# Performance work log

Hardware: AMD Instinct MI355X
Metric: run time of the kernel (lower is better)

The kernel has to match this reference:

```python
import jax, jax.numpy as jnp
import numpy as np

N_NODES = 4096
EDGE_PROB = 0.01


def setup_inputs() -> dict:
    key = jax.random.key(0)
    kx, ka, kw = jax.random.split(key, 3)
    x = jax.random.normal(kx, (4, 32, N_NODES, 12), dtype=jnp.float32)
    u = jax.random.uniform(ka, (N_NODES, N_NODES), dtype=jnp.float32)
    adj = (u < EDGE_PROB).astype(jnp.float32)
    adj = jnp.maximum(adj, adj.T)
    weight = jax.random.normal(kw, (3, 32, 32), dtype=jnp.float32) * 0.1
    bias = jnp.zeros((32,), dtype=jnp.float32)
    return {"x": x, "adj": adj, "weight": weight, "bias": bias}


def reference(x, adj, weight, bias):
    # x: [B, c_in, N, T] -> [B, T, N, c_in] as in AdaptiveGraphConv.forward
    B, C, N, T = x.shape
    h = jnp.transpose(x, (0, 3, 2, 1))  # [B, T, N, C]
    # DenseChebConv (K=3): L = I - D^{-1/2} A D^{-1/2}, inf -> 0 for isolated nodes
    d = adj.sum(axis=-1)
    d_inv_sqrt = jnp.where(d > 0, jnp.where(d > 0, d, 1.0) ** -0.5, 0.0)
    norm_adj = d_inv_sqrt[:, None] * adj * d_inv_sqrt[None, :]
    L = jnp.eye(N, dtype=x.dtype) - norm_adj
    Tx0 = h
    Tx1 = jnp.einsum('mn,btnc->btmc', L, h)
    Tx2 = 2.0 * jnp.einsum('mn,btnc->btmc', L, Tx1) - Tx0
    out = (jnp.einsum('btnc,co->btno', Tx0, weight[0])
           + jnp.einsum('btnc,co->btno', Tx1, weight[1])
           + jnp.einsum('btnc,co->btno', Tx2, weight[2])
           + bias)
    # back to [B, c_out, N, T]
    return jnp.transpose(out, (0, 3, 2, 1))
```

## Files before the change

kernel.cpp:

```cpp
#include <hip/hip_runtime.h>

#define NN 4096
#define CC 32
#define TT 12
#define BB 4
#define BT 48
#define NC 1536
#define MAXD 192
#define FW 512
#define NCH 3
#define STP 36
#define SOP 33

typedef float f32x4 __attribute__((ext_vector_type(4)));
typedef short short8 __attribute__((ext_vector_type(8)));
typedef unsigned short ushort8 __attribute__((ext_vector_type(8)));

__device__ __forceinline__ float bf2f(unsigned short h) {
  return __uint_as_float(((unsigned int)h) << 16);
}
__device__ __forceinline__ unsigned short f2bf(float f) {
  unsigned int u = __float_as_uint(f);
  return (unsigned short)((u + 0x7FFFu + ((u >> 16) & 1u)) >> 16);
}
__device__ __forceinline__ float blo(unsigned int w) { return __uint_as_float(w << 16); }
__device__ __forceinline__ float bhi(unsigned int w) { return __uint_as_float(w & 0xFFFF0000u); }

__global__ __launch_bounds__(256) void k_build(const float* __restrict__ adj,
                                               uint2* __restrict__ edges,
                                               int* __restrict__ deg, float* __restrict__ dis) {
  __shared__ int cnt;
  int m = blockIdx.x;
  if (threadIdx.x == 0) cnt = 0;
  __syncthreads();
  unsigned int* ecol = (unsigned int*)(edges + m * MAXD);
  const uint4* row = (const uint4*)(adj + (size_t)m * NN);
  for (int i = threadIdx.x; i < NN / 4; i += 256) {
    uint4 v = row[i];
    unsigned int ws[4] = {v.x, v.y, v.z, v.w};
    #pragma unroll
    for (int k = 0; k < 4; ++k) {
      if (ws[k] != 0) {
        int p = atomicAdd(&cnt, 1);
        if (p < MAXD) ecol[p * 2] = (unsigned int)(i * 4 + k);
      }
    }
  }
  __syncthreads();
  if (threadIdx.x == 0) {
    int d = cnt < MAXD ? cnt : MAXD;
    deg[m] = d;
    dis[m] = d > 0 ? (float)(1.0 / sqrt((double)d)) : 0.0f;
  }
}

__global__ __launch_bounds__(192) void k_wt(uint2* __restrict__ edges,
                                            const int* __restrict__ deg,
                                            int* __restrict__ degp,
                                            const float* __restrict__ dis) {
  int m = blockIdx.x;
  int j = threadIdx.x;
  int d = deg[m];
  int dp = (d + 15) & ~15;
  if (j < d) {
    unsigned int* e = (unsigned int*)(edges + m * MAXD + j);
    e[1] = __float_as_uint(dis[e[0]]);
  } else if (j < dp) {
    edges[m * MAXD + j] = make_uint2((unsigned int)m, 0u);
  }
  if (j == 0) degp[m] = dp;
}

__global__ __launch_bounds__(256) void k_trans(const float* __restrict__ x,
                                               unsigned short* __restrict__ H) {
  __shared__ unsigned short sT[192 * STP];
  int b = blockIdx.x >> 8;
  int n0 = (blockIdx.x & 255) * 16;
  int c = threadIdx.x >> 3;
  int l8 = threadIdx.x & 7;
  size_t base = ((size_t)(b * CC + c) * NN + n0) * TT;
  #pragma unroll
  for (int it = 0; it < 6; ++it) {
    int j0 = it * 32 + l8 * 4;
    float4 f = *(const float4*)(x + base + j0);
    sT[(j0 + 0) * STP + c] = f2bf(f.x);
    sT[(j0 + 1) * STP + c] = f2bf(f.y);
    sT[(j0 + 2) * STP + c] = f2bf(f.z);
    sT[(j0 + 3) * STP + c] = f2bf(f.w);
  }
  __syncthreads();
  #pragma unroll
  for (int k = 0; k < 6; ++k) {
    int p = (threadIdx.x >> 3) + 32 * k;
    int nl = p / TT, t = p - nl * TT;
    ushort4 v = *(const ushort4*)&sT[p * STP + l8 * 4];
    size_t off = ((size_t)(n0 + nl) * BT + b * TT + t) * CC + l8 * 4;
    *(ushort4*)(H + off) = v;
  }
}

__global__ __launch_bounds__(1024) void k_gather(const unsigned short* __restrict__ S,
                                                 const uint2* __restrict__ edges,
                                                 const int* __restrict__ degp,
                                                 const float* __restrict__ dis,
                                                 unsigned short* __restrict__ D) {
  int tid = threadIdx.x;
  int wid = __builtin_amdgcn_readfirstlane(tid >> 6);
  int lane = tid & 63;
  int m = blockIdx.x * 16 + wid;
  int d = degp[m];
  float dm = dis[m];
  const uint2* ep = edges + (size_t)m * MAXD;
  const unsigned short* Sy = S + blockIdx.y * FW;
  int lo2 = lane * 8;
  float a0 = 0.f, a1 = 0.f, a2 = 0.f, a3 = 0.f;
  float a4 = 0.f, a5 = 0.f, a6 = 0.f, a7 = 0.f;
  for (int e = 0; e < d; e += 8) {
    uint4 hv[8];
    float w[8];
    #pragma unroll
    for (int k = 0; k < 8; ++k) {
      uint2 ew = ep[e + k];
      w[k] = __uint_as_float(ew.y);
      hv[k] = *(const uint4*)(Sy + (int)ew.x * NC + lo2);
    }
    #pragma unroll
    for (int k = 0; k < 8; ++k) {
      float wk = w[k];
      a0 = fmaf(wk, blo(hv[k].x), a0); a1 = fmaf(wk, bhi(hv[k].x), a1);
      a2 = fmaf(wk, blo(hv[k].y), a2); a3 = fmaf(wk, bhi(hv[k].y), a3);
      a4 = fmaf(wk, blo(hv[k].z), a4); a5 = fmaf(wk, bhi(hv[k].z), a5);
      a6 = fmaf(wk, blo(hv[k].w), a6); a7 = fmaf(wk, bhi(hv[k].w), a7);
    }
  }
  int fo = blockIdx.y * FW + lo2;
  ushort8 o;
  o[0] = f2bf(dm * a0); o[1] = f2bf(dm * a1);
  o[2] = f2bf(dm * a2); o[3] = f2bf(dm * a3);
  o[4] = f2bf(dm * a4); o[5] = f2bf(dm * a5);
  o[6] = f2bf(dm * a6); o[7] = f2bf(dm * a7);
  *(ushort8*)(D + (size_t)m * NC + fo) = o;
}

__global__ __launch_bounds__(256) void k_mix(const unsigned short* __restrict__ H,
                                             const unsigned short* __restrict__ G1,
                                             const unsigned short* __restrict__ G2,
                                             const float* __restrict__ W,
                                             const float* __restrict__ bias,
                                             float* __restrict__ out) {
  __shared__ __align__(16) float sOut[192 * SOP];
  int wid = threadIdx.x >> 6, lane = threadIdx.x & 63;
  int lm = lane & 15, quad = lane >> 4;
  short8 bhf[2][3], blf[2][3];
  float bias0[2];
  for (int h = 0; h < 2; ++h)
    for (int g = 0; g < 3; ++g) {
      short8 vh, vl;
      #pragma unroll
      for (int j = 0; j < 8; ++j) {
        int r = quad * 8 + j, c = h * 16 + lm;
        float w0 = W[(0 * CC + r) * CC + c];
        float w1 = W[(1 * CC + r) * CC + c];
        float w2 = W[(2 * CC + r) * CC + c];
        float w = (g == 0) ? (w0 + w1 + w2)
                 : (g == 1) ? (-w1 - 4.f * w2)
                            : (2.f * w2);
        unsigned short hi = f2bf(w);
        vh[j] = (short)hi;
        vl[j] = (short)f2bf(w - bf2f(hi));
      }
      bhf[h][g] = vh; blf[h][g] = vl;
    }
  #pragma unroll
  for (int h = 0; h < 2; ++h) bias0[h] = bias[h * 16 + lm];
  int n0 = blockIdx.x * 4;
  #pragma unroll
  for (int tI = 0; tI < 3; ++tI) {
    int r0l = wid * BT + tI * 16;
    size_t abase = ((size_t)(n0 * BT) + r0l + lm) * CC + quad * 8;
    short8 af0 = *(const short8*)(H + abase);
    short8 af1 = *(const short8*)(G1 + abase);
    short8 af2 = *(const short8*)(G2 + abase);
    #pragma unroll
    for (int h = 0; h < 2; ++h) {
      f32x4 acc = {bias0[h], bias0[h], bias0[h], bias0[h]};
      acc = __builtin_amdgcn_mfma_f32_16x16x32_bf16(af0, bhf[h][0], acc, 0, 0, 0);
      acc = __builtin_amdgcn_mfma_f32_16x16x32_bf16(af0, blf[h][0], acc, 0, 0, 0);
      acc = __builtin_amdgcn_mfma_f32_16x16x32_bf16(af1, bhf[h][1], acc, 0, 0, 0);
      acc = __builtin_amdgcn_mfma_f32_16x16x32_bf16(af1, blf[h][1], acc, 0, 0, 0);
      acc = __builtin_amdgcn_mfma_f32_16x16x32_bf16(af2, bhf[h][2], acc, 0, 0, 0);
      acc = __builtin_amdgcn_mfma_f32_16x16x32_bf16(af2, blf[h][2], acc, 0, 0, 0);
      int o = h * 16 + lm;
      #pragma unroll
      for (int reg = 0; reg < 4; ++reg)
        sOut[(r0l + quad * 4 + reg) * SOP + o] = acc[reg];
    }
  }
  __syncthreads();
  #pragma unroll
  for (int j = 0; j < 6; ++j) {
    int idx = j * 256 + threadIdx.x;
    int bo = idx / 12;
    int fq = idx - bo * 12;
    int p0 = fq * 4;
    float v[4];
    #pragma unroll
    for (int k = 0; k < 4; ++k) {
      int p = p0 + k;
      int nl = p / TT, t = p - nl * TT;
      int b = bo >> 5, o = bo & 31;
      v[k] = sOut[(nl * BT + b * TT + t) * SOP + o];
    }
    size_t base = (((size_t)bo * NN) + n0) * TT + p0;
    *(float4*)(out + base) = make_float4(v[0], v[1], v[2], v[3]);
  }
}

extern "C" void kernel_launch(void* const* d_in, const int* in_sizes, int n_in,
                              void* d_out, int out_size, void* d_ws, size_t ws_size,
                              hipStream_t stream) {
  const float* x    = (const float*)d_in[0];
  const float* adj  = (const float*)d_in[1];
  const float* wgt  = (const float*)d_in[2];
  const float* bias = (const float*)d_in[3];
  char* ws = (char*)d_ws;
  float* dis  = (float*)ws;
  int*   deg  = (int*)(ws + 16384);
  int*   degp = (int*)(ws + 32768);
  uint2* edges = (uint2*)(ws + 49152);
  char* p = ws + 49152 + (size_t)NN * MAXD * 8;
  unsigned short* H  = (unsigned short*)p;
  unsigned short* G1 = (unsigned short*)(p + (size_t)NN * NC * 2);
  unsigned short* G2 = (unsigned short*)(p + (size_t)NN * NC * 4);

  k_build<<<NN, 256, 0, stream>>>(adj, edges, deg, dis);
  k_wt<<<NN, 192, 0, stream>>>(edges, deg, degp, dis);
  k_trans<<<1024, 256, 0, stream>>>(x, H);
  k_gather<<<dim3(NN / 16, NCH), 1024, 0, stream>>>(H, edges, degp, dis, G1);
  k_gather<<<dim3(NN / 16, NCH), 1024, 0, stream>>>(G1, edges, degp, dis, G2);
  k_mix<<<NN / 4, 256, 0, stream>>>(H, G1, G2, wgt, bias, (float*)d_out);
}
```

Measured before the change: 231.8 us.

## Merge adjacency scan and input transpose into one launch with wave-ballot compaction

Folds the adjacency-row scan and the x transpose/bf16 conversion into a single kernel whose blocks split by index into the two jobs. This removes one launch and lets the two independent memory-bound jobs run side by side. The row scan now gives each row to one 64-lane wave and builds the edge list with ballot/popcount prefix sums instead of shared-memory atomics. Edge order becomes deterministic (ascending column), and each row is scanned by one wave instead of a whole block.

Result: slower. 254.4 us (+9.7%).

```diff
diff --git a/kernel.cpp b/kernel.cpp
--- a/kernel.cpp
+++ b/kernel.cpp
@@ -26,31 +26,61 @@
 __device__ __forceinline__ float blo(unsigned int w) { return __uint_as_float(w << 16); }
 __device__ __forceinline__ float bhi(unsigned int w) { return __uint_as_float(w & 0xFFFF0000u); }
 
-__global__ __launch_bounds__(256) void k_build(const float* __restrict__ adj,
-                                               uint2* __restrict__ edges,
-                                               int* __restrict__ deg, float* __restrict__ dis) {
-  __shared__ int cnt;
-  int m = blockIdx.x;
-  if (threadIdx.x == 0) cnt = 0;
-  __syncthreads();
-  unsigned int* ecol = (unsigned int*)(edges + m * MAXD);
-  const uint4* row = (const uint4*)(adj + (size_t)m * NN);
-  for (int i = threadIdx.x; i < NN / 4; i += 256) {
-    uint4 v = row[i];
-    unsigned int ws[4] = {v.x, v.y, v.z, v.w};
-    #pragma unroll
-    for (int k = 0; k < 4; ++k) {
-      if (ws[k] != 0) {
-        int p = atomicAdd(&cnt, 1);
-        if (p < MAXD) ecol[p * 2] = (unsigned int)(i * 4 + k);
+__global__ __launch_bounds__(256) void k_build_trans(const float* __restrict__ adj,
+                                                     const float* __restrict__ x,
+                                                     uint2* __restrict__ edges,
+                                                     int* __restrict__ deg,
+                                                     float* __restrict__ dis,
+                                                     unsigned short* __restrict__ H) {
+  __shared__ unsigned short sT[192 * STP];
+  if (blockIdx.x < 1024) {
+    int wid = threadIdx.x >> 6, lane = threadIdx.x & 63;
+    int m = blockIdx.x * 4 + wid;
+    const float* row = adj + (size_t)m * NN;
+    unsigned int* ecol = (unsigned int*)(edges + m * MAXD);
+    unsigned long long ltmask = (lane == 63) ? ~0ull >> 1
+                                             : (1ull << lane) - 1ull;
+    int base = 0;
+    #pragma unroll 8
+    for (int it = 0; it < 64; ++it) {
+      float v = row[it * 64 + lane];
+      unsigned long long ball = __ballot(v != 0.0f);
+      if (v != 0.0f) {
+        int p = base + __popcll(ball & ltmask);
+        if (p < MAXD) ecol[p * 2] = (unsigned int)(it * 64 + lane);
       }
-    }
-  }
-  __syncthreads();
-  if (threadIdx.x == 0) {
-    int d = cnt < MAXD ? cnt : MAXD;
-    deg[m] = d;
-    dis[m] = d > 0 ? (float)(1.0 / sqrt((double)d)) : 0.0f;
+      base += __popcll(ball);
+    }
+    if (lane == 0) {
+      int d = base < MAXD ? base : MAXD;
+      deg[m] = d;
+      dis[m] = d > 0 ? (float)(1.0 / sqrt((double)d)) : 0.0f;
+    }
+  } else {
+    int bx = blockIdx.x - 1024;
+    int b = bx >> 8;
+    int n0 = (bx & 255) * 16;
+    int c = threadIdx.x >> 3;
+    int l8 = threadIdx.x & 7;
+    size_t base = ((size_t)(b * CC + c) * NN + n0) * TT;
+    #pragma unroll
+    for (int it = 0; it < 6; ++it) {
+      int j0 = it * 32 + l8 * 4;
+      float4 f = *(const float4*)(x + base + j0);
+      sT[(j0 + 0) * STP + c] = f2bf(f.x);
+      sT[(j0 + 1) * STP + c] = f2bf(f.y);
+      sT[(j0 + 2) * STP + c] = f2bf(f.z);
+      sT[(j0 + 3) * STP + c] = f2bf(f.w);
+    }
+    __syncthreads();
+    #pragma unroll
+    for (int k = 0; k < 6; ++k) {
+      int p = (threadIdx.x >> 3) + 32 * k;
+      int nl = p / TT, t = p - nl * TT;
+      ushort4 v = *(const ushort4*)&sT[p * STP + l8 * 4];
+      size_t off = ((size_t)(n0 + nl) * BT + b * TT + t) * CC + l8 * 4;
+      *(ushort4*)(H + off) = v;
+    }
   }
 }
 
@@ -69,34 +99,6 @@
     edges[m * MAXD + j] = make_uint2((unsigned int)m, 0u);
   }
   if (j == 0) degp[m] = dp;
-}
-
-__global__ __launch_bounds__(256) void k_trans(const float* __restrict__ x,
-                                               unsigned short* __restrict__ H) {
-  __shared__ unsigned short sT[192 * STP];
-  int b = blockIdx.x >> 8;
-  int n0 = (blockIdx.x & 255) * 16;
-  int c = threadIdx.x >> 3;
-  int l8 = threadIdx.x & 7;
-  size_t base = ((size_t)(b * CC + c) * NN + n0) * TT;
-  #pragma unroll
-  for (int it = 0; it < 6; ++it) {
-    int j0 = it * 32 + l8 * 4;
-    float4 f = *(const float4*)(x + base + j0);
-    sT[(j0 + 0) * STP + c] = f2bf(f.x);
-    sT[(j0 + 1) * STP + c] = f2bf(f.y);
-    sT[(j0 + 2) * STP + c] = f2bf(f.z);
-    sT[(j0 + 3) * STP + c] = f2bf(f.w);
-  }
-  __syncthreads();
-  #pragma unroll
-  for (int k = 0; k < 6; ++k) {
-    int p = (threadIdx.x >> 3) + 32 * k;
-    int nl = p / TT, t = p - nl * TT;
-    ushort4 v = *(const ushort4*)&sT[p * STP + l8 * 4];
-    size_t off = ((size_t)(n0 + nl) * BT + b * TT + t) * CC + l8 * 4;
-    *(ushort4*)(H + off) = v;
-  }
 }
 
 __global__ __launch_bounds__(1024) void k_gather(const unsigned short* __restrict__ S,
@@ -233,9 +235,8 @@
   unsigned short* G1 = (unsigned short*)(p + (size_t)NN * NC * 2);
   unsigned short* G2 = (unsigned short*)(p + (size_t)NN * NC * 4);
 
-  k_build<<<NN, 256, 0, stream>>>(adj, edges, deg, dis);
+  k_build_trans<<<2048, 256, 0, stream>>>(adj, x, edges, deg, dis, H);
   k_wt<<<NN, 192, 0, stream>>>(edges, deg, degp, dis);
-  k_trans<<<1024, 256, 0, stream>>>(x, H);
   k_gather<<<dim3(NN / 16, NCH), 1024, 0, stream>>>(H, edges, degp, dis, G1);
   k_gather<<<dim3(NN / 16, NCH), 1024, 0, stream>>>(G1, edges, degp, dis, G2);
   k_mix<<<NN / 4, 256, 0, stream>>>(H, G1, G2, wgt, bias, (float*)d_out);
```

## Fuse second gather with channel-mix MFMA and merge build/transpose launches

Applied to the files above, without the earlier changes.

Merges the adjacency-build and input-transpose kernels into one launch, split by block index. Fuses the second sparse gather with the Chebyshev weight-mix MFMA, so each wave keeps its G2 row in shared memory and writes the final output directly. This removes the G2 round-trip through global memory and two launches. In exchange every gather block recomputes the bf16 hi/lo weight fragments, and the output stores become strided per node instead of the previous coalesced transpose through shared memory.

Measured after the change: 302.5 us. 1.3x slower.

```diff
diff --git a/kernel.cpp b/kernel.cpp
--- a/kernel.cpp
+++ b/kernel.cpp
@@ -10,7 +10,6 @@
 #define FW 512
 #define NCH 3
 #define STP 36
-#define SOP 33
 
 typedef float f32x4 __attribute__((ext_vector_type(4)));
 typedef short short8 __attribute__((ext_vector_type(8)));
@@ -26,31 +25,62 @@
 __device__ __forceinline__ float blo(unsigned int w) { return __uint_as_float(w << 16); }
 __device__ __forceinline__ float bhi(unsigned int w) { return __uint_as_float(w & 0xFFFF0000u); }
 
-__global__ __launch_bounds__(256) void k_build(const float* __restrict__ adj,
-                                               uint2* __restrict__ edges,
-                                               int* __restrict__ deg, float* __restrict__ dis) {
+__global__ __launch_bounds__(256) void k_build_trans(const float* __restrict__ adj,
+                                                     const float* __restrict__ x,
+                                                     uint2* __restrict__ edges,
+                                                     int* __restrict__ deg,
+                                                     float* __restrict__ dis,
+                                                     unsigned short* __restrict__ H) {
+  __shared__ unsigned short sT[192 * STP];
   __shared__ int cnt;
-  int m = blockIdx.x;
-  if (threadIdx.x == 0) cnt = 0;
-  __syncthreads();
-  unsigned int* ecol = (unsigned int*)(edges + m * MAXD);
-  const uint4* row = (const uint4*)(adj + (size_t)m * NN);
-  for (int i = threadIdx.x; i < NN / 4; i += 256) {
-    uint4 v = row[i];
-    unsigned int ws[4] = {v.x, v.y, v.z, v.w};
-    #pragma unroll
-    for (int k = 0; k < 4; ++k) {
-      if (ws[k] != 0) {
-        int p = atomicAdd(&cnt, 1);
-        if (p < MAXD) ecol[p * 2] = (unsigned int)(i * 4 + k);
+  if (blockIdx.x < NN) {
+    int m = blockIdx.x;
+    if (threadIdx.x == 0) cnt = 0;
+    __syncthreads();
+    unsigned int* ecol = (unsigned int*)(edges + m * MAXD);
+    const uint4* row = (const uint4*)(adj + (size_t)m * NN);
+    for (int i = threadIdx.x; i < NN / 4; i += 256) {
+      uint4 v = row[i];
+      unsigned int ws[4] = {v.x, v.y, v.z, v.w};
+      #pragma unroll
+      for (int k = 0; k < 4; ++k) {
+        if (ws[k] != 0) {
+          int p = atomicAdd(&cnt, 1);
+          if (p < MAXD) ecol[p * 2] = (unsigned int)(i * 4 + k);
+        }
       }
     }
-  }
-  __syncthreads();
-  if (threadIdx.x == 0) {
-    int d = cnt < MAXD ? cnt : MAXD;
-    deg[m] = d;
-    dis[m] = d > 0 ? (float)(1.0 / sqrt((double)d)) : 0.0f;
+    __syncthreads();
+    if (threadIdx.x == 0) {
+      int d = cnt < MAXD ? cnt : MAXD;
+      deg[m] = d;
+      dis[m] = d > 0 ? (float)(1.0 / sqrt((double)d)) : 0.0f;
+    }
+  } else {
+    int bx = blockIdx.x - NN;
+    int b = bx >> 8;
+    int n0 = (bx & 255) * 16;
+    int c = threadIdx.x >> 3;
+    int l8 = threadIdx.x & 7;
+    size_t base = ((size_t)(b * CC + c) * NN + n0) * TT;
+    #pragma unroll
+    for (int it = 0; it < 6; ++it) {
+      int j0 = it * 32 + l8 * 4;
+      float4 f = *(const float4*)(x + base + j0);
+      sT[(j0 + 0) * STP + c] = f2bf(f.x);
+      sT[(j0 + 1) * STP + c] = f2bf(f.y);
+      sT[(j0 + 2) * STP + c] = f2bf(f.z);
+      sT[(j0 + 3) * STP + c] = f2bf(f.w);
+    }
+    __syncthreads();
+    #pragma unroll
+    for (int k = 0; k < 6; ++k) {
+      int p = (threadIdx.x >> 3) + 32 * k;
+      int nl = p / TT, t = p - nl * TT;
+      ushort4 v = *(const ushort4*)&sT[p * STP + l8 * 4];
+      size_t off = ((size_t)(n0 + nl) * BT + b * TT + t) * CC + l8 * 4;
+      *(ushort4*)(H + off) = v;
+    }
   }
 }
 
@@ -69,34 +99,6 @@
     edges[m * MAXD + j] = make_uint2((unsigned int)m, 0u);
   }
   if (j == 0) degp[m] = dp;
-}
-
-__global__ __launch_bounds__(256) void k_trans(const float* __restrict__ x,
-                                               unsigned short* __restrict__ H) {
-  __shared__ unsigned short sT[192 * STP];
-  int b = blockIdx.x >> 8;
-  int n0 = (blockIdx.x & 255) * 16;
-  int c = threadIdx.x >> 3;
-  int l8 = threadIdx.x & 7;
-  size_t base = ((size_t)(b * CC + c) * NN + n0) * TT;
-  #pragma unroll
-  for (int it = 0; it < 6; ++it) {
-    int j0 = it * 32 + l8 * 4;
-    float4 f = *(const float4*)(x + base + j0);
-    sT[(j0 + 0) * STP + c] = f2bf(f.x);
-    sT[(j0 + 1) * STP + c] = f2bf(f.y);
-    sT[(j0 + 2) * STP + c] = f2bf(f.z);
-    sT[(j0 + 3) * STP + c] = f2bf(f.w);
-  }
-  __syncthreads();
-  #pragma unroll
-  for (int k = 0; k < 6; ++k) {
-    int p = (threadIdx.x >> 3) + 32 * k;
-    int nl = p / TT, t = p - nl * TT;
-    ushort4 v = *(const ushort4*)&sT[p * STP + l8 * 4];
-    size_t off = ((size_t)(n0 + nl) * BT + b * TT + t) * CC + l8 * 4;
-    *(ushort4*)(H + off) = v;
-  }
 }
 
 __global__ __launch_bounds__(1024) void k_gather(const unsigned short* __restrict__ S,
@@ -142,18 +144,65 @@
   *(ushort8*)(D + (size_t)m * NC + fo) = o;
 }
 
-__global__ __launch_bounds__(256) void k_mix(const unsigned short* __restrict__ H,
-                                             const unsigned short* __restrict__ G1,
-                                             const unsigned short* __restrict__ G2,
-                                             const float* __restrict__ W,
-                                             const float* __restrict__ bias,
-                                             float* __restrict__ out) {
-  __shared__ __align__(16) float sOut[192 * SOP];
-  int wid = threadIdx.x >> 6, lane = threadIdx.x & 63;
+__global__ __launch_bounds__(1024, 8) void k_gather_mix(
+    const unsigned short* __restrict__ G1,
+    const unsigned short* __restrict__ H,
+    const uint2* __restrict__ edges,
+    const int* __restrict__ degp,
+    const float* __restrict__ dis,
+    const float* __restrict__ W,
+    const float* __restrict__ bias,
+    float* __restrict__ out) {
+  __shared__ __align__(16) unsigned short sG2[16][16 * CC];
+  int tid = threadIdx.x;
+  int wid = __builtin_amdgcn_readfirstlane(tid >> 6);
+  int lane = tid & 63;
+  int m = blockIdx.x * 16 + wid;
+  int y = blockIdx.y;
+  int d = degp[m];
+  float dm = dis[m];
+  const uint2* ep = edges + (size_t)m * MAXD;
+  const unsigned short* Sy = G1 + y * FW;
+  int lo2 = lane * 8;
+  float a0 = 0.f, a1 = 0.f, a2 = 0.f, a3 = 0.f;
+  float a4 = 0.f, a5 = 0.f, a6 = 0.f, a7 = 0.f;
+  for (int e = 0; e < d; e += 8) {
+    uint4 hv[8];
+    float w[8];
+    #pragma unroll
+    for (int k = 0; k < 8; ++k) {
+      uint2 ew = ep[e + k];
+      w[k] = __uint_as_float(ew.y);
+      hv[k] = *(const uint4*)(Sy + (int)ew.x * NC + lo2);
+    }
+    #pragma unroll
+    for (int k = 0; k < 8; ++k) {
+      float wk = w[k];
+      a0 = fmaf(wk, blo(hv[k].x), a0); a1 = fmaf(wk, bhi(hv[k].x), a1);
+      a2 = fmaf(wk, blo(hv[k].y), a2); a3 = fmaf(wk, bhi(hv[k].y), a3);
+      a4 = fmaf(wk, blo(hv[k].z), a4); a5 = fmaf(wk, bhi(hv[k].z), a5);
+      a6 = fmaf(wk, blo(hv[k].w), a6); a7 = fmaf(wk, bhi(hv[k].w), a7);
+    }
+  }
+  __builtin_amdgcn_sched_barrier(0);
+  ushort8 go;
+  go[0] = f2bf(dm * a0); go[1] = f2bf(dm * a1);
+  go[2] = f2bf(dm * a2); go[3] = f2bf(dm * a3);
+  go[4] = f2bf(dm * a4); go[5] = f2bf(dm * a5);
+  go[6] = f2bf(dm * a6); go[7] = f2bf(dm * a7);
+  *(ushort8*)&sG2[wid][(lane >> 2) * CC + (lane & 3) * 8] = go;
   int lm = lane & 15, quad = lane >> 4;
-  short8 bhf[2][3], blf[2][3];
-  float bias0[2];
-  for (int h = 0; h < 2; ++h)
+  size_t abase = ((size_t)m * BT + y * 16 + lm) * CC + quad * 8;
+  short8 af0 = *(const short8*)(H + abase);
+  short8 af1 = *(const short8*)(G1 + abase);
+  short8 af2 = *(const short8*)&sG2[wid][lm * CC + quad * 8];
+  int bt0 = y * 16 + quad * 4;
+  int b = bt0 / TT, t0 = bt0 - b * TT;
+  #pragma unroll
+  for (int h = 0; h < 2; ++h) {
+    float bs = bias[h * 16 + lm];
+    f32x4 acc = {bs, bs, bs, bs};
+    #pragma unroll
     for (int g = 0; g < 3; ++g) {
       short8 vh, vl;
       #pragma unroll
@@ -169,50 +218,12 @@
         vh[j] = (short)hi;
         vl[j] = (short)f2bf(w - bf2f(hi));
       }
-      bhf[h][g] = vh; blf[h][g] = vl;
-    }
-  #pragma unroll
-  for (int h = 0; h < 2; ++h) bias0[h] = bias[h * 16 + lm];
-  int n0 = blockIdx.x * 4;
-  #pragma unroll
-  for (int tI = 0; tI < 3; ++tI) {
-    int r0l = wid * BT + tI * 16;
-    size_t abase = ((size_t)(n0 * BT) + r0l + lm) * CC + quad * 8;
-    short8 af0 = *(const short8*)(H + abase);
-    short8 af1 = *(const short8*)(G1 + abase);
-    short8 af2 = *(const short8*)(G2 + abase);
-    #pragma unroll
-    for (int h = 0; h < 2; ++h) {
-      f32x4 acc = {bias0[h], bias0[h], bias0[h], bias0[h]};
-      acc = __builtin_amdgcn_mfma_f32_16x16x32_bf16(af0, bhf[h][0], acc, 0, 0, 0);
-      acc = __builtin_amdgcn_mfma_f32_16x16x32_bf16(af0, blf[h][0], acc, 0, 0, 0);
-      acc = __builtin_amdgcn_mfma_f32_16x16x32_bf16(af1, bhf[h][1], acc, 0, 0, 0);
-      acc = __builtin_amdgcn_mfma_f32_16x16x32_bf16(af1, blf[h][1], acc, 0, 0, 0);
-      acc = __builtin_amdgcn_mfma_f32_16x16x32_bf16(af2, bhf[h][2], acc, 0, 0, 0);
-      acc = __builtin_amdgcn_mfma_f32_16x16x32_bf16(af2, blf[h][2], acc, 0, 0, 0);
-      int o = h * 16 + lm;
-      #pragma unroll
-      for (int reg = 0; reg < 4; ++reg)
-        sOut[(r0l + quad * 4 + reg) * SOP + o] = acc[reg];
-    }
-  }
-  __syncthreads();
-  #pragma unroll
-  for (int j = 0; j < 6; ++j) {
-    int idx = j * 256 + threadIdx.x;
-    int bo = idx / 12;
-    int fq = idx - bo * 12;
-    int p0 = fq * 4;
-    float v[4];
-    #pragma unroll
-    for (int k = 0; k < 4; ++k) {
-      int p = p0 + k;
-      int nl = p / TT, t = p - nl * TT;
-      int b = bo >> 5, o = bo & 31;
-      v[k] = sOut[(nl * BT + b * TT + t) * SOP + o];
-    }
-    size_t base = (((size_t)bo * NN) + n0) * TT + p0;
-    *(float4*)(out + base) = make_float4(v[0], v[1], v[2], v[3]);
+      short8 af = (g == 0) ? af0 : (g == 1) ? af1 : af2;
+      acc = __builtin_amdgcn_mfma_f32_16x16x32_bf16(af, vh, acc, 0, 0, 0);
+      acc = __builtin_amdgcn_mfma_f32_16x16x32_bf16(af, vl, acc, 0, 0, 0);
+    }
+    int o = h * 16 + lm;
+    *(f32x4*)(out + ((size_t)(b * CC + o) * NN + m) * TT + t0) = acc;
   }
 }
 
@@ -231,12 +242,10 @@
   char* p = ws + 49152 + (size_t)NN * MAXD * 8;
   unsigned short* H  = (unsigned short*)p;
   unsigned short* G1 = (unsigned short*)(p + (size_t)NN * NC * 2);
-  unsigned short* G2 = (unsigned short*)(p + (size_t)NN * NC * 4);
-
-  k_build<<<NN, 256, 0, stream>>>(adj, edges, deg, dis);
+
+  k_build_trans<<<NN + 1024, 256, 0, stream>>>(adj, x, edges, deg, dis, H);
   k_wt<<<NN, 192, 0, stream>>>(edges, deg, degp, dis);
-  k_trans<<<1024, 256, 0, stream>>>(x, H);
   k_gather<<<dim3(NN / 16, NCH), 1024, 0, stream>>>(H, edges, degp, dis, G1);
-  k_gather<<<dim3(NN / 16, NCH), 1024, 0, stream>>>(G1, edges, degp, dis, G2);
-  k_mix<<<NN / 4, 256, 0, stream>>>(H, G1, G2, wgt, bias, (float*)d_out);
-}
+  k_gather_mix<<<dim3(NN / 16, NCH), 1024, 0, stream>>>(G1, H, edges, degp, dis,
+                                                        wgt, bias, (float*)d_out);
+}
```
